# Kernel tuning notes

Measured on AMD Instinct MI355X. Metric: run time of the kernel, lower is better.

## Reference

```python
import jax, jax.numpy as jnp
import numpy as np

B, T, WIN, HID = 256, 16384, 5, 5  # hidden must equal window for mse_loss shapes to match


def setup_inputs() -> dict:
    key = jax.random.key(0)
    k1, k2, k3 = jax.random.split(key, 3)
    series = jax.random.normal(k1, (B, T), dtype=jnp.float32)
    # nn.Linear(window_size, hidden_size) params: weight [H, W], bias [H]
    bound = 1.0 / np.sqrt(WIN)
    weight = jax.random.uniform(k2, (HID, WIN), jnp.float32, -bound, bound)
    bias = jax.random.uniform(k3, (HID,), jnp.float32, -bound, bound)
    threshold = jnp.float32(0.1)  # change_point_threshold parameter
    return {"series": series, "weight": weight, "bias": bias, "threshold": threshold}


def reference(series, weight, bias, threshold):
    Bb, Tt = series.shape
    H, Wd = weight.shape
    N = Tt - Wd  # number of windows = time_steps - window_size
    # Gather all sliding windows at once: idx [N, W]
    idx = jnp.arange(N)[:, None] + jnp.arange(Wd)[None, :]
    local = series[:, idx]        # [B, N, W]  == series[:, i:i+W] for all i
    target = series[:, idx + 1]   # [B, N, W]  == series[:, i+1:i+W+1]
    # Tiny per-window linear, batched over all windows
    transformed = jnp.einsum('bnw,hw->bnh', local, weight) + bias  # [B, N, H]
    # F.mse_loss reduces over all elements (B and H) per window
    losses = jnp.mean((transformed - target) ** 2, axis=(0, 2))    # [N]
    # change-point logic vectorized: diff of consecutive losses vs threshold
    diffs = jnp.abs(losses[1:] - losses[:-1])                      # [N-1]
    change_mask = diffs > threshold                                # [N-1] bool
    return losses, diffs, change_mask
```

## Files before the change

### kernel.cpp

```cpp
#include <hip/hip_runtime.h>

#define BB    256
#define TT    16384
#define WIN   5
#define HID   5
#define NN    (TT - WIN)
#define TILE  32
#define NT    512
#define SROWS 64
#define NCOLS (TILE + WIN + 1)
#define LDSW  41

__global__ __launch_bounds__(256)
void llsa_fused(const float* __restrict__ series,
                const float* __restrict__ weight,
                const float* __restrict__ bias,
                const float* __restrict__ thr_ptr,
                float* __restrict__ out) {
    const int tid  = threadIdx.x;
    const int n0   = blockIdx.x * TILE;
    const int c    = tid & (TILE - 1);
    const int rsub = tid >> 5;

    float w[HID][WIN], bi[HID];
#pragma unroll
    for (int h = 0; h < HID; ++h) {
        bi[h] = bias[h];
#pragma unroll
        for (int v = 0; v < WIN; ++v) w[h][v] = weight[h * WIN + v];
    }

    __shared__ float lds[SROWS * LDSW];
    __shared__ float psum[8 * TILE];
    __shared__ float Ls[TILE + 1];

    float acc  = 0.f;
    float bacc = 0.f;

    for (int stage = 0; stage < BB / SROWS; ++stage) {
        const int b0 = stage * SROWS;
        __syncthreads();
        for (int idx = tid; idx < SROWS * NCOLS; idx += 256) {
            const int r   = idx / NCOLS;
            const int cc  = idx - r * NCOLS;
            const int col = n0 + cc;
            float v = (col < TT) ? series[(size_t)(b0 + r) * TT + col] : 0.f;
            lds[r * LDSW + cc] = v;
        }
        __syncthreads();

#pragma unroll
        for (int k = 0; k < 8; ++k) {
            const float* row = &lds[(rsub * 8 + k) * LDSW + c];
            float sv[WIN + 1];
#pragma unroll
            for (int j = 0; j <= WIN; ++j) sv[j] = row[j];
#pragma unroll
            for (int h = 0; h < HID; ++h) {
                float t = bi[h];
#pragma unroll
                for (int v = 0; v < WIN; ++v) t = fmaf(sv[v], w[h][v], t);
                const float e = t - sv[h + 1];
                acc = fmaf(e, e, acc);
            }
        }

        if (tid < SROWS) {
            const float* row = &lds[tid * LDSW + TILE];
            float sv[WIN + 1];
#pragma unroll
            for (int j = 0; j <= WIN; ++j) sv[j] = row[j];
#pragma unroll
            for (int h = 0; h < HID; ++h) {
                float t = bi[h];
#pragma unroll
                for (int v = 0; v < WIN; ++v) t = fmaf(sv[v], w[h][v], t);
                const float e = t - sv[h + 1];
                bacc = fmaf(e, e, bacc);
            }
        }
    }

    float bs = bacc;
#pragma unroll
    for (int off = 32; off >= 1; off >>= 1) bs += __shfl_down(bs, off);

    psum[rsub * TILE + c] = acc;
    __syncthreads();

    const float inv = 1.0f / (float)(BB * HID);
    if (tid == 0) Ls[TILE] = bs * inv;
    if (tid < TILE) {
        float s = 0.f;
#pragma unroll
        for (int g = 0; g < 8; ++g) s += psum[g * TILE + tid];
        Ls[tid] = s * inv;
    }
    __syncthreads();

    if (tid < TILE) {
        const int i = n0 + tid;
        if (i < NN) {
            const float li = Ls[tid];
            out[i] = li;
            if (i < NN - 1) {
                const float d = fabsf(Ls[tid + 1] - li);
                out[NN + i] = d;
                out[2 * NN - 1 + i] = (d > thr_ptr[0]) ? 1.0f : 0.0f;
            }
        }
    }
}

extern "C" void kernel_launch(void* const* d_in, const int* in_sizes, int n_in,
                              void* d_out, int out_size, void* d_ws, size_t ws_size,
                              hipStream_t stream) {
    const float* series = (const float*)d_in[0];
    const float* weight = (const float*)d_in[1];
    const float* bias   = (const float*)d_in[2];
    const float* thr    = (const float*)d_in[3];
    float* out = (float*)d_out;
    (void)d_ws; (void)ws_size; (void)in_sizes; (void)n_in; (void)out_size;

    llsa_fused<<<NT, 256, 0, stream>>>(series, weight, bias, thr, out);
}
```

Baseline: 85.99 us.

## Load full batch tile into LDS once with float4 loads and remap blocks

Replaces the four-stage loop (64 rows per stage, scalar strided loads, two barriers per stage) with a single load of all 256 rows into LDS, using float4 vector loads for the 32-column body and per-thread scalar loads for the halo. Block indices are permuted so consecutive block IDs map to tiles 64 apart. The compute loop processes two rows at a time with independent accumulators to add ILP. This uses roughly 45KB of LDS per block, which may limit occupancy. The float4 reads assume n0 + c4 is 16-byte aligned.

```diff
diff --git a/kernel.cpp b/kernel.cpp
--- a/kernel.cpp
+++ b/kernel.cpp
@@ -7,9 +7,8 @@
 #define NN    (TT - WIN)
 #define TILE  32
 #define NT    512
-#define SROWS 64
 #define NCOLS (TILE + WIN + 1)
-#define LDSW  41
+#define LDSW  44
 
 __global__ __launch_bounds__(256)
 void llsa_fused(const float* __restrict__ series,
@@ -17,10 +16,9 @@
                 const float* __restrict__ bias,
                 const float* __restrict__ thr_ptr,
                 float* __restrict__ out) {
-    const int tid  = threadIdx.x;
-    const int n0   = blockIdx.x * TILE;
-    const int c    = tid & (TILE - 1);
-    const int rsub = tid >> 5;
+    const int tid = threadIdx.x;
+    const int t  = (blockIdx.x & 7) * 64 + (blockIdx.x >> 3);
+    const int n0 = t * TILE;
 
     float w[HID][WIN], bi[HID];
 #pragma unroll
@@ -30,57 +28,74 @@
         for (int v = 0; v < WIN; ++v) w[h][v] = weight[h * WIN + v];
     }
 
-    __shared__ float lds[SROWS * LDSW];
+    __shared__ float lds[BB * LDSW];
     __shared__ float psum[8 * TILE];
     __shared__ float Ls[TILE + 1];
 
-    float acc  = 0.f;
+    {
+        const int c4 = (tid & 7) * 4;
+        const int rb = tid >> 3;
+#pragma unroll
+        for (int it = 0; it < 8; ++it) {
+            const int r = it * 32 + rb;
+            const float4 v = *(const float4*)(series + (size_t)r * TT + n0 + c4);
+            *(float4*)(&lds[r * LDSW + c4]) = v;
+        }
+    }
+    {
+        const float* row = series + (size_t)tid * TT;
+#pragma unroll
+        for (int j = 0; j < WIN + 1; ++j) {
+            const int col = n0 + TILE + j;
+            lds[tid * LDSW + TILE + j] = (col < TT) ? row[col] : 0.f;
+        }
+    }
+    __syncthreads();
+
+    const int c    = tid & (TILE - 1);
+    const int rsub = tid >> 5;
+    float ax = 0.f, ay = 0.f;
+#pragma unroll
+    for (int k = 0; k < 32; k += 2) {
+        const float* rA = &lds[(rsub * 32 + k) * LDSW + c];
+        const float* rB = rA + LDSW;
+        float sx[WIN + 1], sy[WIN + 1];
+#pragma unroll
+        for (int j = 0; j <= WIN; ++j) { sx[j] = rA[j]; sy[j] = rB[j]; }
+#pragma unroll
+        for (int h = 0; h < HID; ++h) {
+            float tx = bi[h], ty = bi[h];
+#pragma unroll
+            for (int v = 0; v < WIN; ++v) {
+                tx = fmaf(sx[v], w[h][v], tx);
+                ty = fmaf(sy[v], w[h][v], ty);
+            }
+            const float ex = tx - sx[h + 1];
+            const float ey = ty - sy[h + 1];
+            ax = fmaf(ex, ex, ax);
+            ay = fmaf(ey, ey, ay);
+        }
+    }
+    const float acc = ax + ay;
+
     float bacc = 0.f;
-
-    for (int stage = 0; stage < BB / SROWS; ++stage) {
-        const int b0 = stage * SROWS;
-        __syncthreads();
-        for (int idx = tid; idx < SROWS * NCOLS; idx += 256) {
-            const int r   = idx / NCOLS;
-            const int cc  = idx - r * NCOLS;
-            const int col = n0 + cc;
-            float v = (col < TT) ? series[(size_t)(b0 + r) * TT + col] : 0.f;
-            lds[r * LDSW + cc] = v;
-        }
-        __syncthreads();
-
+    if (tid < 64) {
 #pragma unroll
-        for (int k = 0; k < 8; ++k) {
-            const float* row = &lds[(rsub * 8 + k) * LDSW + c];
+        for (int s = 0; s < 4; ++s) {
+            const float* row = &lds[(tid + 64 * s) * LDSW + TILE];
             float sv[WIN + 1];
 #pragma unroll
             for (int j = 0; j <= WIN; ++j) sv[j] = row[j];
 #pragma unroll
             for (int h = 0; h < HID; ++h) {
-                float t = bi[h];
+                float tt = bi[h];
 #pragma unroll
-                for (int v = 0; v < WIN; ++v) t = fmaf(sv[v], w[h][v], t);
-                const float e = t - sv[h + 1];
-                acc = fmaf(e, e, acc);
-            }
-        }
-
-        if (tid < SROWS) {
-            const float* row = &lds[tid * LDSW + TILE];
-            float sv[WIN + 1];
-#pragma unroll
-            for (int j = 0; j <= WIN; ++j) sv[j] = row[j];
-#pragma unroll
-            for (int h = 0; h < HID; ++h) {
-                float t = bi[h];
-#pragma unroll
-                for (int v = 0; v < WIN; ++v) t = fmaf(sv[v], w[h][v], t);
-                const float e = t - sv[h + 1];
+                for (int v = 0; v < WIN; ++v) tt = fmaf(sv[v], w[h][v], tt);
+                const float e = tt - sv[h + 1];
                 bacc = fmaf(e, e, bacc);
             }
         }
     }
-
     float bs = bacc;
 #pragma unroll
     for (int off = 32; off >= 1; off >>= 1) bs += __shfl_down(bs, off);
```

After: 75.24 us. 12.5% less time.
